# Performance work log

Hardware: AMD Instinct MI355X
Metric: run time of the kernel (lower is better)

The kernel has to match this reference:

```python
import jax, jax.numpy as jnp
import numpy as np

N = 100000
NS = 16
C_IN = 64
C_MID = 64   # mid_planes = out_planes // 1
C_OUT = 64
S = 8        # share_planes
BN_EPS = 1e-5


def _bn(x, g, b):
    # eval-mode BatchNorm1d with running_mean=0, running_var=1
    return x * (g / jnp.sqrt(1.0 + BN_EPS)) + b


def setup_inputs() -> dict:
    key = jax.random.key(0)
    ks = jax.random.split(key, 16)
    def lin(k, fan_in, fan_out):
        bound = 1.0 / np.sqrt(fan_in)
        kw, kb = jax.random.split(k)
        W = jax.random.uniform(kw, (fan_in, fan_out), jnp.float32, -bound, bound)
        b = jax.random.uniform(kb, (fan_out,), jnp.float32, -bound, bound)
        return W, b
    p = jax.random.normal(ks[0], (N, 3), jnp.float32)
    x = jax.random.normal(ks[1], (N, C_IN), jnp.float32)
    idx = jax.random.randint(ks[2], (N, NS), 0, N, jnp.int32)
    Wq, bq = lin(ks[3], C_IN, C_MID)
    Wk, bk = lin(ks[4], C_IN, C_MID)
    Wv, bv = lin(ks[5], C_IN, C_OUT)
    Wp1, bp1 = lin(ks[6], 3, 3)
    gp = jnp.ones((3,), jnp.float32); bp = jnp.zeros((3,), jnp.float32)
    Wp2, bp2 = lin(ks[7], 3, C_OUT)
    g1 = jnp.ones((C_MID,), jnp.float32); bb1 = jnp.zeros((C_MID,), jnp.float32)
    Wa, ba = lin(ks[8], C_MID, C_MID // S)
    g2 = jnp.ones((C_MID // S,), jnp.float32); bb2 = jnp.zeros((C_MID // S,), jnp.float32)
    Wb, bw = lin(ks[9], C_OUT // S, C_OUT // S)
    return dict(p=p, x=x, idx=idx, Wq=Wq, bq=bq, Wk=Wk, bk=bk, Wv=Wv, bv=bv,
                Wp1=Wp1, bp1=bp1, gp=gp, bp=bp, Wp2=Wp2, bp2=bp2,
                g1=g1, bb1=bb1, Wa=Wa, ba=ba, g2=g2, bb2=bb2, Wb=Wb, bw=bw)


def reference(p, x, idx, Wq, bq, Wk, bk, Wv, bv, Wp1, bp1, gp, bp, Wp2, bp2,
              g1, bb1, Wa, ba, g2, bb2, Wb, bw):
    # QKV encoding
    x_q = x @ Wq + bq                      # [N, mid]
    x_k = x @ Wk + bk                      # [N, mid]
    x_v = x @ Wv + bv                      # [N, out]
    # KNN gather (queryandgroup with precomputed neighbor indices)
    xk_g = x_k[idx]                        # [N, ns, mid]
    xv_g = x_v[idx]                        # [N, ns, out]
    p_r = p[idx] - p[:, None, :]           # [N, ns, 3] relative coords
    # Positional encoding MLP: Linear(3,3) -> BN -> ReLU -> Linear(3,out)
    pe = jax.nn.relu(_bn(p_r @ Wp1 + bp1, gp, bp)) @ Wp2 + bp2   # [N, ns, out]
    # Relation: diff-based scores (+ pos enc; out//mid == 1 so sum(2) is identity)
    w = xk_g - x_q[:, None, :] + pe        # [N, ns, mid]
    # linear_w: BN -> ReLU -> Linear(mid, mid/s) -> BN -> ReLU -> Linear(mid/s, mid/s)
    w = jax.nn.relu(_bn(w, g1, bb1)) @ Wa + ba
    w = jax.nn.relu(_bn(w, g2, bb2)) @ Wb + bw                   # [N, ns, out/s]
    w = jax.nn.softmax(w, axis=1)          # softmax over neighbor axis
    # Value aggregation with shared attention planes
    v = (xv_g + pe).reshape(N, NS, S, C_OUT // S)
    out = (v * w[:, :, None, :]).sum(axis=1).reshape(N, C_OUT)
    return out
```

## Files before the change

### kernel.cpp

```cpp
#include <hip/hip_runtime.h>
#include <hip/hip_bf16.h>

typedef unsigned int u32;
typedef unsigned short u16;
typedef __attribute__((ext_vector_type(8))) short short8;
typedef __attribute__((ext_vector_type(4))) float f32x4;
typedef __attribute__((ext_vector_type(2))) float f32x2;
typedef __attribute__((ext_vector_type(4))) u32 u32x4;

#define N_PTS 100000
#define NSAMP 16

__device__ __forceinline__ float lo2f(u32 u){ return __uint_as_float(u << 16); }
__device__ __forceinline__ float hi2f(u32 u){ return __uint_as_float(u & 0xffff0000u); }
__device__ __forceinline__ float us2f(u16 u){ return __uint_as_float(((u32)u) << 16); }

__device__ __forceinline__ u16 f2bf(float f) {
    u32 u = __float_as_uint(f);
    return (u16)((u + 0x7fffu + ((u >> 16) & 1u)) >> 16);
}
__device__ __forceinline__ u32 pack2(float k, float v) {
    return (u32)f2bf(k) | ((u32)f2bf(v) << 16);
}

#define WAVE_LDS_FENCE() asm volatile("s_waitcnt lgkmcnt(0)" ::: "memory")

__device__ __forceinline__ bool detect_f32(const u16* __restrict__ xprobe) {
    float f = us2f(xprobe[(threadIdx.x & 63) * 2]);
    int cnt = __syncthreads_count(fabsf(f) > 1024.0f ? 1 : 0);
    return cnt >= 8;
}

__device__ __forceinline__ float rawf(const void* s, int i, bool isf32) {
    return isf32 ? ((const float*)s)[i] : us2f(((const u16*)s)[i]);
}

#define OFF_WP1  0
#define OFF_BP1  12
#define OFF_GP   16
#define OFF_BP   20
#define OFF_WP2  24
#define OFF_BP2  216
#define OFF_G1   280
#define OFF_BB1  344
#define OFF_BA   408
#define OFF_G2   416
#define OFF_BB2  424
#define OFF_BW   432
#define OFF_WAT  448
#define OFF_WBT  960
#define CW_PAD   4096

#define QKV_TPB 10
__global__ __launch_bounds__(256) void qkv_mfma_kernel(
    const u16* __restrict__ xraw,
    const void* s0,  const void* s1,  const void* s2,  const void* s3,
    const void* s4,  const void* s5,  const void* s6,  const void* s7,
    const void* s8,  const void* s9,  const void* s10, const void* s11,
    const void* s12, const void* s13, const void* s14, const void* s15,
    const void* s16, const void* s17, const void* s18, const void* s19,
    float* __restrict__ cw,
    float* __restrict__ Q, u32* __restrict__ KV)
{
    bool isf32 = detect_f32(xraw);
    const int w   = threadIdx.x >> 6;
    const int l   = threadIdx.x & 63;
    const int col = l & 15;
    const int g   = l >> 4;

    if (blockIdx.x == 0) {
        const void* srcs[12] = {s6,s7,s8,s9,s10,s11,s12,s13,s15,s16,s17,s19};
        const int   sizes[12]= {9,3,3,3,192,64,64,64,8,8,8,8};
        const int   offs[12] = {OFF_WP1,OFF_BP1,OFF_GP,OFF_BP,OFF_WP2,OFF_BP2,
                                OFF_G1,OFF_BB1,OFF_BA,OFF_G2,OFF_BB2,OFF_BW};
        int tid = threadIdx.x;
        for (int a = 0; a < 12; a++)
            for (int k = tid; k < sizes[a]; k += 256)
                cw[offs[a] + k] = rawf(srcs[a], k, isf32);
        for (int t = tid; t < 512 + 64; t += 256) {
            if (t < 512) {
                int s = t >> 6, cc = t & 63;
                cw[OFF_WAT + s * 64 + cc] = rawf(s14, cc * 8 + s, isf32);
            } else {
                int r = t - 512;
                int tt = r >> 3, ss = r & 7;
                cw[OFF_WBT + tt * 8 + ss] = rawf(s18, ss * 8 + tt, isf32);
            }
        }
    }

    const void* wsrc[3] = {s0, s2, s4};
    short8 bh[3][2], bl[3][2];
#pragma unroll
    for (int m = 0; m < 3; m++)
#pragma unroll
        for (int kh = 0; kh < 2; kh++)
#pragma unroll
            for (int j = 0; j < 8; j++) {
                float wv_ = rawf(wsrc[m], (kh * 32 + g * 8 + j) * 64 + w * 16 + col, isf32);
                u16 hb = f2bf(wv_);
                bh[m][kh][j] = (short)hb;
                bl[m][kh][j] = (short)f2bf(wv_ - us2f(hb));
            }
    float bq[4], bk[4], bv[4];
#pragma unroll
    for (int r = 0; r < 4; r++) {
        bq[r] = rawf(s1, w * 16 + g * 4 + r, isf32);
        bk[r] = rawf(s3, w * 16 + g * 4 + r, isf32);
        bv[r] = rawf(s5, w * 16 + g * 4 + r, isf32);
    }

#define LOAD_A(IT, AH, AL)                                                        \
    {                                                                             \
        const int M0_ = (blockIdx.x * QKV_TPB + (IT)) * 16;                       \
        if (isf32) {                                                              \
            const float4* xf = (const float4*)xraw;                               \
            _Pragma("unroll")                                                     \
            for (int kh = 0; kh < 2; kh++) {                                      \
                float4 f0 = xf[(size_t)(M0_ + col) * 16 + kh * 8 + g * 2];        \
                float4 f1 = xf[(size_t)(M0_ + col) * 16 + kh * 8 + g * 2 + 1];    \
                float ff[8] = {f0.x, f0.y, f0.z, f0.w, f1.x, f1.y, f1.z, f1.w};   \
                _Pragma("unroll")                                                 \
                for (int j = 0; j < 8; j++) {                                     \
                    u16 hb_ = f2bf(ff[j]);                                        \
                    AH[kh][j] = (short)hb_;                                       \
                    AL[kh][j] = (short)f2bf(ff[j] - us2f(hb_));                   \
                }                                                                 \
            }                                                                     \
        } else {                                                                  \
            const short8* xb = (const short8*)xraw;                               \
            _Pragma("unroll")                                                     \
            for (int kh = 0; kh < 2; kh++)                                        \
                AH[kh] = xb[(size_t)(M0_ + col) * 8 + kh * 4 + g];                \
        }                                                                         \
    }

    short8 ahA[2], alA[2], ahB[2], alB[2];
    LOAD_A(0, ahA, alA);

#pragma unroll
    for (int it = 0; it < QKV_TPB; it++) {
        short8 (&ah)[2] = (it & 1) ? ahB : ahA;
        short8 (&al)[2] = (it & 1) ? alB : alA;
        short8 (&ahN)[2] = (it & 1) ? ahA : ahB;
        short8 (&alN)[2] = (it & 1) ? alA : alB;
        if (it + 1 < QKV_TPB) LOAD_A(it + 1, ahN, alN);

        const int M0 = (blockIdx.x * QKV_TPB + it) * 16;
        f32x4 aQ = {bq[0], bq[1], bq[2], bq[3]};
        f32x4 aK = {bk[0], bk[1], bk[2], bk[3]};
        f32x4 aV = {bv[0], bv[1], bv[2], bv[3]};

#pragma unroll
        for (int kh = 0; kh < 2; kh++) {
            aQ = __builtin_amdgcn_mfma_f32_16x16x32_bf16(bh[0][kh], ah[kh], aQ, 0, 0, 0);
            aK = __builtin_amdgcn_mfma_f32_16x16x32_bf16(bh[1][kh], ah[kh], aK, 0, 0, 0);
            aV = __builtin_amdgcn_mfma_f32_16x16x32_bf16(bh[2][kh], ah[kh], aV, 0, 0, 0);
            aQ = __builtin_amdgcn_mfma_f32_16x16x32_bf16(bl[0][kh], ah[kh], aQ, 0, 0, 0);
            aK = __builtin_amdgcn_mfma_f32_16x16x32_bf16(bl[1][kh], ah[kh], aK, 0, 0, 0);
            aV = __builtin_amdgcn_mfma_f32_16x16x32_bf16(bl[2][kh], ah[kh], aV, 0, 0, 0);
            if (isf32) {
                aQ = __builtin_amdgcn_mfma_f32_16x16x32_bf16(bh[0][kh], al[kh], aQ, 0, 0, 0);
                aK = __builtin_amdgcn_mfma_f32_16x16x32_bf16(bh[1][kh], al[kh], aK, 0, 0, 0);
                aV = __builtin_amdgcn_mfma_f32_16x16x32_bf16(bh[2][kh], al[kh], aV, 0, 0, 0);
            }
        }

        {
            const int row = M0 + col;
            float4 qv = {aQ[0], aQ[1], aQ[2], aQ[3]};
            *(float4*)&Q[(size_t)row * 64 + w * 16 + g * 4] = qv;
            u32x4 kvv = {pack2(aK[0], aV[0]), pack2(aK[1], aV[1]),
                         pack2(aK[2], aV[2]), pack2(aK[3], aV[3])};
            *(u32x4*)&KV[(size_t)row * 64 + w * 16 + g * 4] = kvv;
        }
    }
#undef LOAD_A
}

__global__ __launch_bounds__(256, 4) void attn_kernel(
    const u16* __restrict__ P, const int* __restrict__ IDX,
    const u16* __restrict__ xprobe, const float* __restrict__ cw,
    const float* __restrict__ Q, const u32* __restrict__ KV,
    void* __restrict__ OUT)
{
    __shared__ __align__(16) float wvbuf[8][NSAMP * 68];
    __shared__ __align__(16) float tbbuf[8][NSAMP * 8];

    bool isf32 = detect_f32(xprobe);

    const int pt  = threadIdx.x >> 6;
    const int c   = threadIdx.x & 63;
    const int i0  = blockIdx.x * 8 + pt * 2;
    const int i1  = i0 + 1;
    const int sl0 = pt * 2, sl1 = sl0 + 1;
    const float rs = 1.0f / sqrtf(1.0f + 1e-5f);

    float* hb0 = &tbbuf[sl0][0];
    float* hb1 = &tbbuf[sl1][0];
    float* w20 = &wvbuf[sl0][0];
    float* w21 = &wvbuf[sl1][0];

    const int jv0 = IDX[(size_t)i0 * NSAMP + (c & 15)];
    const int jv1 = IDX[(size_t)i1 * NSAMP + (c & 15)];

    u32 kv0[NSAMP], kv1[NSAMP];
    const u32* KVc = KV + c;
#pragma unroll
    for (int n = 0; n < NSAMP; n++) {
        int j = __builtin_amdgcn_readlane(jv0, n);
        kv0[n] = KVc[(size_t)j << 6];
    }
#pragma unroll
    for (int n = 0; n < NSAMP; n++) {
        int j = __builtin_amdgcn_readlane(jv1, n);
        kv1[n] = KVc[(size_t)j << 6];
    }

    const float qq0 = Q[(size_t)i0 * 64 + c];
    const float qq1 = Q[(size_t)i1 * 64 + c];

    const float* Pf = (const float*)P;
    const int n_p  = c / 3;
    const int d_p  = c - n_p * 3;
    const int np15 = n_p & 15;
    const int jp0  = __shfl(jv0, np15, 64);
    const int jp1  = __shfl(jv1, np15, 64);
    float pj0, pj1, pid0, pid1;
    if (isf32) {
        pj0 = Pf[(size_t)jp0 * 3 + d_p];  pid0 = Pf[(size_t)i0 * 3 + d_p];
        pj1 = Pf[(size_t)jp1 * 3 + d_p];  pid1 = Pf[(size_t)i1 * 3 + d_p];
    } else {
        pj0 = us2f(P[(size_t)jp0 * 3 + d_p]);  pid0 = us2f(P[(size_t)i0 * 3 + d_p]);
        pj1 = us2f(P[(size_t)jp1 * 3 + d_p]);  pid1 = us2f(P[(size_t)i1 * 3 + d_p]);
    }
    const float pr0 = pj0 - pid0, pr1 = pj1 - pid1;
    const int lb = np15 * 3;
    const float pA0 = __shfl(pr0, lb + 0, 64);
    const float pA1 = __shfl(pr0, lb + 1, 64);
    const float pA2 = __shfl(pr0, lb + 2, 64);
    const float pB0 = __shfl(pr1, lb + 0, 64);
    const float pB1 = __shfl(pr1, lb + 1, 64);
    const float pB2 = __shfl(pr1, lb + 2, 64);
    {
        float gd  = cw[OFF_GP + d_p] * rs;
        float w0s = cw[OFF_WP1 + 0 * 3 + d_p] * gd;
        float w1s = cw[OFF_WP1 + 1 * 3 + d_p] * gd;
        float w2s = cw[OFF_WP1 + 2 * 3 + d_p] * gd;
        float bs  = cw[OFF_BP1 + d_p] * gd + cw[OFF_BP + d_p];
        float hA = fmaxf(fmaf(pA2, w2s, fmaf(pA1, w1s, fmaf(pA0, w0s, bs))), 0.0f);
        float hB = fmaxf(fmaf(pB2, w2s, fmaf(pB1, w1s, fmaf(pB0, w0s, bs))), 0.0f);
        if (c < 48) {
            hb0[np15 * 4 + d_p] = hA;
            hb1[np15 * 4 + d_p] = hB;
        }
    }
    WAVE_LDS_FENCE();

    const float wp2c0 = cw[OFF_WP2 + 0 * 64 + c];
    const float wp2c1 = cw[OFF_WP2 + 1 * 64 + c];
    const float wp2c2 = cw[OFF_WP2 + 2 * 64 + c];
    const float bp2c  = cw[OFF_BP2 + c];
    const float g1c   = cw[OFF_G1  + c] * rs;
    const float bb1c  = cw[OFF_BB1 + c];

    float pv0[NSAMP], pv1[NSAMP];

#pragma unroll
    for (int n = 0; n < NSAMP; n++) {
        float4 hb = *((const float4*)&hb0[n * 4]);
        float pe = fmaf(hb.z, wp2c2, fmaf(hb.y, wp2c1, fmaf(hb.x, wp2c0, bp2c)));
        float kk = lo2f(kv0[n]);
        float vv = hi2f(kv0[n]);
        wvbuf[sl0][n * 68 + c] = fmaxf(fmaf(kk - qq0 + pe, g1c, bb1c), 0.0f);
        pv0[n] = vv + pe;
    }
#pragma unroll
    for (int n = 0; n < NSAMP; n++) {
        float4 hb = *((const float4*)&hb1[n * 4]);
        float pe = fmaf(hb.z, wp2c2, fmaf(hb.y, wp2c1, fmaf(hb.x, wp2c0, bp2c)));
        float kk = lo2f(kv1[n]);
        float vv = hi2f(kv1[n]);
        wvbuf[sl1][n * 68 + c] = fmaxf(fmaf(kk - qq1 + pe, g1c, bb1c), 0.0f);
        pv1[n] = vv + pe;
    }
    __syncthreads();

    const int s2s = c & 7, s2n = c >> 3;
    f32x2 aA0 = {cw[OFF_BA + s2s], 0.0f};
    f32x2 aA1 = aA0, aB0 = aA0, aB1 = aA0;
    const float4* waT4 = (const float4*)(cw + OFF_WAT + s2s * 64);
#pragma unroll
    for (int c4 = 0; c4 < 16; c4++) {
        float4 wa = waT4[c4];
        f32x2 waA = {wa.x, wa.y}, waB = {wa.z, wa.w};
        float4 rA0 = *((const float4*)&wvbuf[sl0][s2n * 68 + c4 * 4]);
        float4 rA1 = *((const float4*)&wvbuf[sl0][(s2n + 8) * 68 + c4 * 4]);
        float4 rB0 = *((const float4*)&wvbuf[sl1][s2n * 68 + c4 * 4]);
        float4 rB1 = *((const float4*)&wvbuf[sl1][(s2n + 8) * 68 + c4 * 4]);
        f32x2 tA0a = {rA0.x, rA0.y}, tA0b = {rA0.z, rA0.w};
        f32x2 tA1a = {rA1.x, rA1.y}, tA1b = {rA1.z, rA1.w};
        f32x2 tB0a = {rB0.x, rB0.y}, tB0b = {rB0.z, rB0.w};
        f32x2 tB1a = {rB1.x, rB1.y}, tB1b = {rB1.z, rB1.w};
        aA0 += tA0a * waA;  aA0 += tA0b * waB;
        aA1 += tA1a * waA;  aA1 += tA1b * waB;
        aB0 += tB0a * waA;  aB0 += tB0b * waB;
        aB1 += tB1a * waA;  aB1 += tB1b * waB;
    }
    {
        float g2s = cw[OFF_G2 + s2s] * rs, bb2s = cw[OFF_BB2 + s2s];
        tbbuf[sl0][s2n * 8 + s2s]       = fmaxf(fmaf(aA0.x + aA0.y, g2s, bb2s), 0.0f);
        tbbuf[sl0][(s2n + 8) * 8 + s2s] = fmaxf(fmaf(aA1.x + aA1.y, g2s, bb2s), 0.0f);
        tbbuf[sl1][s2n * 8 + s2s]       = fmaxf(fmaf(aB0.x + aB0.y, g2s, bb2s), 0.0f);
        tbbuf[sl1][(s2n + 8) * 8 + s2s] = fmaxf(fmaf(aB1.x + aB1.y, g2s, bb2s), 0.0f);
    }
    __syncthreads();

    f32x2 wA0 = {cw[OFF_BW + s2s], 0.0f};
    f32x2 wA1 = wA0, wB0 = wA0, wB1 = wA0;
    {
        float4 wb0 = *(const float4*)(cw + OFF_WBT + s2s * 8);
        float4 wb1 = *(const float4*)(cw + OFF_WBT + s2s * 8 + 4);
        f32x2 b0 = {wb0.x, wb0.y}, b1 = {wb0.z, wb0.w};
        f32x2 b2 = {wb1.x, wb1.y}, b3 = {wb1.z, wb1.w};
#define ACC_LOGIT(ACC, SL, ROW)                                                   \
        {                                                                         \
            float4 t0_ = *((const float4*)&tbbuf[SL][(ROW) * 8]);                 \
            float4 t1_ = *((const float4*)&tbbuf[SL][(ROW) * 8 + 4]);             \
            f32x2 u0_ = {t0_.x, t0_.y}, u1_ = {t0_.z, t0_.w};                     \
            f32x2 u2_ = {t1_.x, t1_.y}, u3_ = {t1_.z, t1_.w};                     \
            ACC += u0_ * b0;  ACC += u1_ * b1;  ACC += u2_ * b2;  ACC += u3_ * b3;\
        }
        ACC_LOGIT(wA0, sl0, s2n)
        ACC_LOGIT(wA1, sl0, s2n + 8)
        ACC_LOGIT(wB0, sl1, s2n)
        ACC_LOGIT(wB1, sl1, s2n + 8)
#undef ACC_LOGIT
    }
    float lA0 = wA0.x + wA0.y, lA1 = wA1.x + wA1.y;
    float lB0 = wB0.x + wB0.y, lB1 = wB1.x + wB1.y;

    {
        float m0 = fmaxf(lA0, lA1);
        m0 = fmaxf(m0, __shfl_xor(m0, 8, 64));
        m0 = fmaxf(m0, __shfl_xor(m0, 16, 64));
        m0 = fmaxf(m0, __shfl_xor(m0, 32, 64));
        float e00 = __expf(lA0 - m0), e01 = __expf(lA1 - m0);
        float s0 = e00 + e01;
        s0 += __shfl_xor(s0, 8, 64);
        s0 += __shfl_xor(s0, 16, 64);
        s0 += __shfl_xor(s0, 32, 64);
        float inv0 = 1.0f / s0;
        w20[s2n * 8 + s2s]       = e00 * inv0;
        w20[(s2n + 8) * 8 + s2s] = e01 * inv0;

        float m1 = fmaxf(lB0, lB1);
        m1 = fmaxf(m1, __shfl_xor(m1, 8, 64));
        m1 = fmaxf(m1, __shfl_xor(m1, 16, 64));
        m1 = fmaxf(m1, __shfl_xor(m1, 32, 64));
        float e10 = __expf(lB0 - m1), e11 = __expf(lB1 - m1);
        float s1 = e10 + e11;
        s1 += __shfl_xor(s1, 8, 64);
        s1 += __shfl_xor(s1, 16, 64);
        s1 += __shfl_xor(s1, 32, 64);
        float inv1 = 1.0f / s1;
        w21[s2n * 8 + s2s]       = e10 * inv1;
        w21[(s2n + 8) * 8 + s2s] = e11 * inv1;
    }
    __syncthreads();

    f32x2 ov0 = {0.0f, 0.0f}, ov1 = {0.0f, 0.0f};
#pragma unroll
    for (int n = 0; n < NSAMP; n += 2) {
        f32x2 p0 = {pv0[n], pv0[n + 1]};
        f32x2 w0 = {w20[n * 8 + s2s], w20[(n + 1) * 8 + s2s]};
        f32x2 p1 = {pv1[n], pv1[n + 1]};
        f32x2 w1 = {w21[n * 8 + s2s], w21[(n + 1) * 8 + s2s]};
        ov0 += p0 * w0;
        ov1 += p1 * w1;
    }
    float o0 = ov0.x + ov0.y;
    float o1 = ov1.x + ov1.y;
    if (isf32) {
        ((float*)OUT)[(size_t)i0 * 64 + c] = o0;
        ((float*)OUT)[(size_t)i1 * 64 + c] = o1;
    } else {
        ((__hip_bfloat16*)OUT)[(size_t)i0 * 64 + c] = __float2bfloat16(o0);
        ((__hip_bfloat16*)OUT)[(size_t)i1 * 64 + c] = __float2bfloat16(o1);
    }
}

extern "C" void kernel_launch(void* const* d_in, const int* in_sizes, int n_in,
                              void* d_out, int out_size, void* d_ws, size_t ws_size,
                              hipStream_t stream)
{
    const u16* p   = (const u16*)d_in[0];
    const u16* x   = (const u16*)d_in[1];
    const int* idx = (const int*)d_in[2];

    float* cw = (float*)d_ws;
    float* Q  = cw + CW_PAD;
    u32*   KV = (u32*)(Q + (size_t)N_PTS * 64);

    qkv_mfma_kernel<<<625, 256, 0, stream>>>(
        x,
        d_in[3],  d_in[4],  d_in[5],  d_in[6],  d_in[7],  d_in[8],
        d_in[9],  d_in[10], d_in[11], d_in[12], d_in[13], d_in[14],
        d_in[15], d_in[16], d_in[17], d_in[18], d_in[19], d_in[20],
        d_in[21], d_in[22], cw, Q, KV);
    attn_kernel<<<N_PTS / 8, 256, 0, stream>>>(p, idx, x, cw, Q, KV, d_out);
}
```

Baseline: 281.5 us.

## Store attention intermediate in LDS as bf16 and raise launch-bounds occupancy

The post-BN/ReLU relation tensor staged in shared memory is now stored as bf16 instead of fp32, halving the wvbuf LDS footprint and the read traffic in the Wa projection. The launch bounds hint goes from 4 to 6 blocks per SM so more blocks can be resident. The cost is extra convert instructions on write and read, lost precision in the intermediate, and register pressure from the tighter occupancy target. The w20/w21 pointers are recast to float over the bf16 buffer, so any unseen code using them may now index wrongly.

```diff
diff --git a/kernel.cpp b/kernel.cpp
--- a/kernel.cpp
+++ b/kernel.cpp
@@ -4,6 +4,7 @@
 typedef unsigned int u32;
 typedef unsigned short u16;
 typedef __attribute__((ext_vector_type(8))) short short8;
+typedef __attribute__((ext_vector_type(4))) short short4v;
 typedef __attribute__((ext_vector_type(4))) float f32x4;
 typedef __attribute__((ext_vector_type(2))) float f32x2;
 typedef __attribute__((ext_vector_type(4))) u32 u32x4;
@@ -178,13 +179,13 @@
 #undef LOAD_A
 }
 
-__global__ __launch_bounds__(256, 4) void attn_kernel(
+__global__ __launch_bounds__(256, 6) void attn_kernel(
     const u16* __restrict__ P, const int* __restrict__ IDX,
     const u16* __restrict__ xprobe, const float* __restrict__ cw,
     const float* __restrict__ Q, const u32* __restrict__ KV,
     void* __restrict__ OUT)
 {
-    __shared__ __align__(16) float wvbuf[8][NSAMP * 68];
+    __shared__ __align__(16) u16   wvbufh[8][NSAMP * 68];
     __shared__ __align__(16) float tbbuf[8][NSAMP * 8];
 
     bool isf32 = detect_f32(xprobe);
@@ -198,8 +199,8 @@
 
     float* hb0 = &tbbuf[sl0][0];
     float* hb1 = &tbbuf[sl1][0];
-    float* w20 = &wvbuf[sl0][0];
-    float* w21 = &wvbuf[sl1][0];
+    float* w20 = (float*)&wvbufh[sl0][0];
+    float* w21 = (float*)&wvbufh[sl1][0];
 
     const int jv0 = IDX[(size_t)i0 * NSAMP + (c & 15)];
     const int jv1 = IDX[(size_t)i1 * NSAMP + (c & 15)];
@@ -272,7 +273,7 @@
         float pe = fmaf(hb.z, wp2c2, fmaf(hb.y, wp2c1, fmaf(hb.x, wp2c0, bp2c)));
         float kk = lo2f(kv0[n]);
         float vv = hi2f(kv0[n]);
-        wvbuf[sl0][n * 68 + c] = fmaxf(fmaf(kk - qq0 + pe, g1c, bb1c), 0.0f);
+        wvbufh[sl0][n * 68 + c] = f2bf(fmaxf(fmaf(kk - qq0 + pe, g1c, bb1c), 0.0f));
         pv0[n] = vv + pe;
     }
 #pragma unroll
@@ -281,7 +282,7 @@
         float pe = fmaf(hb.z, wp2c2, fmaf(hb.y, wp2c1, fmaf(hb.x, wp2c0, bp2c)));
         float kk = lo2f(kv1[n]);
         float vv = hi2f(kv1[n]);
-        wvbuf[sl1][n * 68 + c] = fmaxf(fmaf(kk - qq1 + pe, g1c, bb1c), 0.0f);
+        wvbufh[sl1][n * 68 + c] = f2bf(fmaxf(fmaf(kk - qq1 + pe, g1c, bb1c), 0.0f));
         pv1[n] = vv + pe;
     }
     __syncthreads();
@@ -294,14 +295,18 @@
     for (int c4 = 0; c4 < 16; c4++) {
         float4 wa = waT4[c4];
         f32x2 waA = {wa.x, wa.y}, waB = {wa.z, wa.w};
-        float4 rA0 = *((const float4*)&wvbuf[sl0][s2n * 68 + c4 * 4]);
-        float4 rA1 = *((const float4*)&wvbuf[sl0][(s2n + 8) * 68 + c4 * 4]);
-        float4 rB0 = *((const float4*)&wvbuf[sl1][s2n * 68 + c4 * 4]);
-        float4 rB1 = *((const float4*)&wvbuf[sl1][(s2n + 8) * 68 + c4 * 4]);
-        f32x2 tA0a = {rA0.x, rA0.y}, tA0b = {rA0.z, rA0.w};
-        f32x2 tA1a = {rA1.x, rA1.y}, tA1b = {rA1.z, rA1.w};
-        f32x2 tB0a = {rB0.x, rB0.y}, tB0b = {rB0.z, rB0.w};
-        f32x2 tB1a = {rB1.x, rB1.y}, tB1b = {rB1.z, rB1.w};
+        short4v hA0 = *((const short4v*)&wvbufh[sl0][s2n * 68 + c4 * 4]);
+        short4v hA1 = *((const short4v*)&wvbufh[sl0][(s2n + 8) * 68 + c4 * 4]);
+        short4v hB0 = *((const short4v*)&wvbufh[sl1][s2n * 68 + c4 * 4]);
+        short4v hB1 = *((const short4v*)&wvbufh[sl1][(s2n + 8) * 68 + c4 * 4]);
+        f32x2 tA0a = {us2f((u16)hA0.x), us2f((u16)hA0.y)};
+        f32x2 tA0b = {us2f((u16)hA0.z), us2f((u16)hA0.w)};
+        f32x2 tA1a = {us2f((u16)hA1.x), us2f((u16)hA1.y)};
+        f32x2 tA1b = {us2f((u16)hA1.z), us2f((u16)hA1.w)};
+        f32x2 tB0a = {us2f((u16)hB0.x), us2f((u16)hB0.y)};
+        f32x2 tB0b = {us2f((u16)hB0.z), us2f((u16)hB0.w)};
+        f32x2 tB1a = {us2f((u16)hB1.x), us2f((u16)hB1.y)};
+        f32x2 tB1b = {us2f((u16)hB1.z), us2f((u16)hB1.w)};
         aA0 += tA0a * waA;  aA0 += tA0b * waB;
         aA1 += tA1a * waA;  aA1 += tA1b * waB;
         aB0 += tB0a * waA;  aB0 += tB0b * waB;
```

New measurement: 336.3 us. 1.19x slower.
